# Kernel optimization log

Hardware: AMD Instinct MI355X
Metric: run time of the kernel (lower is better)

The kernel has to match this reference:

```python
import jax, jax.numpy as jnp
import numpy as np


def _ln(z, g, b, eps=1e-5):
    mu = z.mean(-1, keepdims=True)
    v = ((z - mu) ** 2).mean(-1, keepdims=True)
    return (z - mu) / jnp.sqrt(v + eps) * g + b


def _forward(x, C_prev, n_prev, m_prev, ln_in_g, ln_in_b, wq, bq, wk, bk, wv, bv, wi, bi, wf, bf, wo, bo, rd_w1, rd_b1, rd_g, rd_be, rd_w2, rd_b2, ssm_log_lam, ssm_log_b, ssm_c, ssm_log_d, ssm_log_step, ssm_vol_gate, ssm_alpha, ssm_ln_g, ssm_ln_b, ln_mem_g, ln_mem_b):
    B, S, F = x.shape
    D = wq.shape[0]
    sqd = jnp.sqrt(jnp.float32(D))
    w = max(1, int(S * 0.2))
    pad0 = jnp.zeros((B, 1, F), x.dtype)
    cs = jnp.concatenate([pad0, jnp.cumsum(x, 1)], 1)
    cs2 = jnp.concatenate([pad0, jnp.cumsum(x * x, 1)], 1)
    wsum = cs[:, w:] - cs[:, :-w]
    wsq = cs2[:, w:] - cs2[:, :-w]
    var = (wsq - wsum * wsum / w) / (w - 1)
    std = jnp.sqrt(jnp.clip(var, 0.0))
    vol = jnp.concatenate([jnp.broadcast_to(std[:, :1], (B, w - 1, F)), std], 1)
    sv = vol.mean(2, keepdims=True)
    sv = sv / (sv.mean(1, keepdims=True) + 1e-6)  # [B,S,1]
    # --- parallel gate computation ---
    xn = _ln(x, ln_in_g, ln_in_b)
    regime = jax.nn.softmax(jax.nn.gelu(_ln(xn @ rd_w1.T + rd_b1, rd_g, rd_be), approximate=False) @ rd_w2.T + rd_b2, axis=-1)
    q = xn @ wq.T + bq
    k = (xn @ wk.T + bk) / sqd
    v = xn @ wv.T + bv
    it = xn @ wi.T + bi  # [B,S,1]
    ft = xn @ wf.T + bf
    o = jax.nn.sigmoid(xn @ wo.T + bo)
    # --- stabilize_gates (running-max exponential stabilization) ---
    mp = jnp.clip(m_prev, -100.0, 100.0)[:, None, :]  # [B,1,1]
    m_t = jnp.maximum(ft, mp + ft)
    ig = jnp.exp(jnp.clip(it - m_t, -15.0, 15.0))
    fg = jnp.exp(jnp.clip(ft + mp - m_t, -15.0, 15.0))
    # --- store_key_value outer products + cumulative matrix memory ---
    kn = k / (jnp.linalg.norm(k, axis=2, keepdims=True) + 1e-12) * sqd
    vn = v / (jnp.linalg.norm(v, axis=2, keepdims=True) + 1e-6) * sqd
    upd = jnp.clip(ig, 0.0, 1.0)[..., None] * (vn[..., :, None] * kn[..., None, :])  # [B,S,D,D]
    f_cum = jnp.cumprod(fg, axis=1)  # [B,S,1]
    C_t = f_cum[..., None] * C_prev[:, None] + jnp.cumsum(upd, 1)
    # --- structured state-space mixing, vectorized over the D memory rows ---
    lam = -jnp.exp(ssm_log_lam)
    step = jnp.exp(ssm_log_step)
    a_disc = (2.0 + step * lam) / (2.0 - step * lam)  # bilinear discretization
    b_disc = step * (1.0 + a_disc) * jnp.exp(ssm_log_b)[:, 0] / 2.0
    xr = C_t.transpose(0, 2, 1, 3).reshape(B * D, S, D)  # rows folded into batch
    volr = jnp.broadcast_to(sv[:, None, :, 0], (B, D, S)).reshape(B * D, S)
    u = xr.mean(-1)  # [BD,S], per-step scalar drive
    vgate = jax.nn.sigmoid(ssm_vol_gate)
    def stepf(h, inp):
        u_t, vol_t = inp
        h = a_disc[None] * h + b_disc[None] * u_t[:, None]
        h = _ln(h, ssm_ln_g, ssm_ln_b)
        h = h / (1.0 + vgate[None] * vol_t[:, None])
        return h, h
    h0 = jnp.zeros((B * D, D), x.dtype)
    _, hs = jax.lax.scan(stepf, h0, (u.T, volr.T))  # [S,BD,D]
    yscal = jnp.einsum('sbn,n->bs', hs, ssm_c[0])  # [BD,S]
    y = yscal[..., None] + jnp.exp(ssm_log_d) * xr
    alpha = jax.nn.sigmoid(ssm_alpha)
    mixed = alpha * xr + (1.0 - alpha) * y
    C_mixed = mixed.reshape(B, D, S, D).transpose(0, 2, 1, 3)
    mf = regime[:, :, 0:1][..., None]  # regime-aware mixing factor
    C_t = C_mixed * mf + C_t * (1.0 - mf)
    C_t = C_t / (jnp.linalg.norm(C_t.reshape(B, S, D * D), axis=-1)[..., None, None] + 1e-6) * sqd
    # --- mLSTM readout (stabilizer_threshold = 1.0) ---
    n_t = f_cum * n_prev[:, None, :] + jnp.cumsum(ig * k, 1)
    h_til = jnp.einsum('bsij,bsj->bsi', C_t, q)
    denom = jnp.maximum(jnp.abs(jnp.sum(n_t * q, -1, keepdims=True)), 1.0)
    return o * _ln(h_til / denom, ln_mem_g, ln_mem_b)


def setup_inputs() -> dict:
    key = jax.random.key(0)
    ks = jax.random.split(key, 12)
    B, S, F, D = 8, 512, 32, 64
    sF, sD = 1.0 / np.sqrt(F), 1.0 / np.sqrt(D)
    n = lambda k, sh, s=1.0: jax.random.normal(k, sh, jnp.float32) * s
    return dict(
        x=n(ks[0], (B, S, F)),
        C_prev=jnp.zeros((B, D, D), jnp.float32),
        n_prev=jnp.zeros((B, D), jnp.float32),
        m_prev=jnp.zeros((B, 1), jnp.float32),
        ln_in_g=jnp.ones((F,), jnp.float32), ln_in_b=jnp.zeros((F,), jnp.float32),
        wq=n(ks[1], (D, F), sF), bq=jnp.zeros((D,), jnp.float32),
        wk=n(ks[2], (D, F), sF), bk=jnp.zeros((D,), jnp.float32),
        wv=n(ks[3], (D, F), sF), bv=jnp.zeros((D,), jnp.float32),
        wi=n(ks[4], (1, F), sF), bi=jnp.zeros((1,), jnp.float32),
        wf=n(ks[5], (1, F), sF), bf=jnp.ones((1,), jnp.float32),
        wo=n(ks[6], (D, F), sF), bo=jnp.zeros((D,), jnp.float32),
        rd_w1=n(ks[7], (D, F), sF), rd_b1=jnp.zeros((D,), jnp.float32),
        rd_g=jnp.ones((D,), jnp.float32), rd_be=jnp.zeros((D,), jnp.float32),
        rd_w2=n(ks[8], (4, D), sD), rd_b2=jnp.zeros((4,), jnp.float32),
        ssm_log_lam=jnp.linspace(np.log(0.001), np.log(0.1), D).astype(jnp.float32),
        ssm_log_b=jax.random.uniform(ks[9], (D, 1), jnp.float32, -0.5, 0.5),
        ssm_c=n(ks[10], (1, D), sD),
        ssm_log_d=jnp.zeros((1,), jnp.float32),
        ssm_log_step=jnp.float32(np.log(0.001)),
        ssm_vol_gate=jnp.ones((D,), jnp.float32),
        ssm_alpha=jnp.float32(0.7),
        ssm_ln_g=jnp.ones((D,), jnp.float32), ssm_ln_b=jnp.zeros((D,), jnp.float32),
        ln_mem_g=jnp.ones((D,), jnp.float32), ln_mem_b=jnp.zeros((D,), jnp.float32),
    )


def reference(x, C_prev, n_prev, m_prev, ln_in_g, ln_in_b, wq, bq, wk, bk, wv, bv, wi, bi, wf, bf, wo, bo, rd_w1, rd_b1, rd_g, rd_be, rd_w2, rd_b2, ssm_log_lam, ssm_log_b, ssm_c, ssm_log_d, ssm_log_step, ssm_vol_gate, ssm_alpha, ssm_ln_g, ssm_ln_b, ln_mem_g, ln_mem_b):
    return _forward(x, C_prev, n_prev, m_prev, ln_in_g, ln_in_b, wq, bq, wk, bk, wv, bv, wi, bi, wf, bf, wo, bo, rd_w1, rd_b1, rd_g, rd_be, rd_w2, rd_b2, ssm_log_lam, ssm_log_b, ssm_c, ssm_log_d, ssm_log_step, ssm_vol_gate, ssm_alpha, ssm_ln_g, ssm_ln_b, ln_mem_g, ln_mem_b)
```

## Files before the change

kernel.cpp:

```cpp
#include <hip/hip_runtime.h>
#include <math.h>

#define BB 8
#define SS 512
#define FF 32
#define DD 64
#define WVOL 102
#define CH 16
#define NCH (SS / CH)

template<int CTRL, int RM, bool BC>
__device__ __forceinline__ float updpp(float oldv, float x) {
  return __int_as_float(__builtin_amdgcn_update_dpp(
      __float_as_int(oldv), __float_as_int(x), CTRL, RM, 0xF, BC));
}
__device__ __forceinline__ float rlane(float v, int l) {
  return __int_as_float(__builtin_amdgcn_readlane(__float_as_int(v), l));
}
__device__ __forceinline__ float dsum64(float x) {
  x += updpp<0x111, 0xF, true>(0.f, x);
  x += updpp<0x112, 0xF, true>(0.f, x);
  x += updpp<0x114, 0xF, true>(0.f, x);
  x += updpp<0x118, 0xF, true>(0.f, x);
  x += updpp<0x142, 0xF, true>(0.f, x);
  x += updpp<0x143, 0xF, true>(0.f, x);
  return rlane(x, 63);
}
__device__ __forceinline__ float dsum32(float x) {
  x += updpp<0x111, 0xF, true>(0.f, x);
  x += updpp<0x112, 0xF, true>(0.f, x);
  x += updpp<0x114, 0xF, true>(0.f, x);
  x += updpp<0x118, 0xF, true>(0.f, x);
  x += updpp<0x142, 0xF, true>(0.f, x);
  return rlane(x, 31);
}
__device__ __forceinline__ float dsum16(float x) {
  x += updpp<0x111, 0xF, true>(0.f, x);
  x += updpp<0x112, 0xF, true>(0.f, x);
  x += updpp<0x114, 0xF, true>(0.f, x);
  x += updpp<0x118, 0xF, true>(0.f, x);
  return x;
}
__device__ __forceinline__ float dscan_add(float x) {
  x += updpp<0x111, 0xF, true>(0.f, x);
  x += updpp<0x112, 0xF, true>(0.f, x);
  x += updpp<0x114, 0xF, true>(0.f, x);
  x += updpp<0x118, 0xF, true>(0.f, x);
  x += updpp<0x142, 0xA, true>(0.f, x);
  x += updpp<0x143, 0xC, true>(0.f, x);
  return x;
}
__device__ __forceinline__ float dscan_mul(float x) {
  x *= updpp<0x111, 0xF, false>(1.f, x);
  x *= updpp<0x112, 0xF, false>(1.f, x);
  x *= updpp<0x114, 0xF, false>(1.f, x);
  x *= updpp<0x118, 0xF, false>(1.f, x);
  x *= updpp<0x142, 0xA, false>(1.f, x);
  x *= updpp<0x143, 0xC, false>(1.f, x);
  return x;
}

__global__ void k_prep(const float* __restrict__ Cp,
                       const float* __restrict__ wq, const float* __restrict__ wk,
                       const float* __restrict__ wv, const float* __restrict__ wo,
                       const float* __restrict__ rw1,
                       float* __restrict__ CpT, float* __restrict__ wqT,
                       float* __restrict__ wkT, float* __restrict__ wvT,
                       float* __restrict__ woT, float* __restrict__ rw1T,
                       float* __restrict__ cpr, float* __restrict__ cpn2) {
  int blk = blockIdx.x; int lane = threadIdx.x;
  if (blk < BB) {
    int b = blk;
    const float* rowp = Cp + (size_t)(b * DD + lane) * DD;
    float rs = 0.f, r2 = 0.f;
#pragma unroll 8
    for (int j = 0; j < DD; ++j) {
      float c = rowp[j];
      rs += c; r2 = fmaf(c, c, r2);
      CpT[(size_t)(b * DD + j) * DD + lane] = c;
    }
    cpr[b * DD + lane] = rs;
    float tot2 = dsum64(r2);
    if (lane == 0) cpn2[b] = tot2;
  } else {
    const float* src; float* dst;
    switch (blk - BB) {
      case 0: src = wq;  dst = wqT;  break;
      case 1: src = wk;  dst = wkT;  break;
      case 2: src = wv;  dst = wvT;  break;
      case 3: src = wo;  dst = woT;  break;
      default: src = rw1; dst = rw1T; break;
    }
#pragma unroll 8
    for (int f = 0; f < FF; ++f) dst[f * DD + lane] = src[lane * FF + f];
  }
}

__global__ void k_vol_std(const float* __restrict__ x, float* __restrict__ svraw) {
  int b = blockIdx.x; int s = WVOL - 1 + blockIdx.y;
  int lane = threadIdx.x; int f = lane & 31; int half = lane >> 5;
  const float* xb = x + (size_t)(b * SS) * FF + f;
  float wsum = 0.f, wsq = 0.f;
  int t0 = s - WVOL + 1 + half;
#pragma unroll 17
  for (int k = 0; k < WVOL / 2; ++k) {
    float xv = xb[(t0 + 2 * k) * FF];
    wsum += xv; wsq = fmaf(xv, xv, wsq);
  }
  wsum += __shfl_xor(wsum, 32); wsq += __shfl_xor(wsq, 32);
  float var = (wsq - wsum * wsum * (1.f / WVOL)) * (1.f / (WVOL - 1));
  float sd = sqrtf(fmaxf(var, 0.f));
  float m = dsum64(sd) * 0.5f * (1.f / FF);
  if (lane == 0) svraw[b * SS + s] = m;
}

__global__ void k_proj(const float* __restrict__ x, const float* __restrict__ m_prev,
                       const float* __restrict__ CpT,
                       const float* __restrict__ ln_in_g, const float* __restrict__ ln_in_b,
                       const float* __restrict__ wqT, const float* __restrict__ bq,
                       const float* __restrict__ wkT, const float* __restrict__ bk,
                       const float* __restrict__ wvT, const float* __restrict__ bv,
                       const float* __restrict__ wi, const float* __restrict__ bi,
                       const float* __restrict__ wf, const float* __restrict__ bf,
                       const float* __restrict__ woT, const float* __restrict__ bo,
                       const float* __restrict__ rw1T, const float* __restrict__ rd_b1,
                       const float* __restrict__ rd_g, const float* __restrict__ rd_be,
                       const float* __restrict__ rd_w2, const float* __restrict__ rd_b2,
                       float* __restrict__ qo, float* __restrict__ kno, float* __restrict__ vno,
                       float* __restrict__ iko, float* __restrict__ oo,
                       float* __restrict__ cg_a, float* __restrict__ fg_a,
                       float* __restrict__ mf_a, float* __restrict__ cks_a,
                       float* __restrict__ qsum_a, float* __restrict__ zc) {
  int bs = blockIdx.x; int b = bs / SS;
  int lane = threadIdx.x;
  __shared__ float xs[FF];
  __shared__ float ks[DD];
  float xv = (lane < FF) ? x[bs * FF + lane] : 0.f;
  float s1x = dsum32(xv);
  float s2x = dsum32(xv * xv);
  if (lane < FF) {
    float mu = s1x * (1.f / FF);
    float var = s2x * (1.f / FF) - mu * mu;
    xs[lane] = (xv - mu) * rsqrtf(var + 1e-5f) * ln_in_g[lane] + ln_in_b[lane];
  }
  __syncthreads();
  int d = lane;
  float aq = bq[d], ak = bk[d], av = bv[d], ao = bo[d], at = rd_b1[d];
#pragma unroll
  for (int f = 0; f < FF; ++f) {
    float xf = xs[f];
    aq = fmaf(xf, wqT[f * DD + d], aq);
    ak = fmaf(xf, wkT[f * DD + d], ak);
    av = fmaf(xf, wvT[f * DD + d], av);
    ao = fmaf(xf, woT[f * DD + d], ao);
    at = fmaf(xf, rw1T[f * DD + d], at);
  }
  float pit = (lane < FF) ? xs[lane] * wi[lane] : 0.f;
  float pft = (lane < FF) ? xs[lane] * wf[lane] : 0.f;
  float itv = dsum32(pit) + bi[0];
  float ftv = dsum32(pft) + bf[0];
  float s1 = dsum64(at), s2 = dsum64(at * at);
  float mu = s1 * (1.f / DD);
  float var = s2 * (1.f / DD) - mu * mu;
  float tn = (at - mu) * rsqrtf(var + 1e-5f) * rd_g[d] + rd_be[d];
  float ge = 0.5f * tn * (1.f + erff(tn * 0.70710678118654752f));
  float l0 = dsum64(ge * rd_w2[0 * DD + d]) + rd_b2[0];
  float l1 = dsum64(ge * rd_w2[1 * DD + d]) + rd_b2[1];
  float l2 = dsum64(ge * rd_w2[2 * DD + d]) + rd_b2[2];
  float l3 = dsum64(ge * rd_w2[3 * DD + d]) + rd_b2[3];
  float mx = fmaxf(fmaxf(l0, l1), fmaxf(l2, l3));
  float e0 = expf(l0 - mx), e1 = expf(l1 - mx), e2 = expf(l2 - mx), e3 = expf(l3 - mx);
  float mfv = e0 / (e0 + e1 + e2 + e3);
  float kd = ak * 0.125f;
  float kk = dsum64(kd * kd);
  float knd = kd * (8.f / (sqrtf(kk) + 1e-12f));
  float vv = dsum64(av * av);
  float vnd = av * (8.f / (sqrtf(vv) + 1e-6f));
  float ksum = dsum64(knd);
  float qsum = dsum64(aq);
  float mp = fminf(fmaxf(m_prev[b], -100.f), 100.f);
  float mt = fmaxf(ftv, mp + ftv);
  float ig = expf(fminf(fmaxf(itv - mt, -15.f), 15.f));
  float fg = expf(fminf(fmaxf(ftv + mp - mt, -15.f), 15.f));
  float cg = fminf(ig, 1.f);
  qo[bs * DD + d] = aq;
  kno[bs * DD + d] = knd;
  vno[bs * DD + d] = vnd;
  iko[bs * DD + d] = ig * kd;
  oo[bs * DD + d] = 1.f / (1.f + expf(-ao));
  ks[d] = knd;
  __syncthreads();
  float acc = 0.f;
  const float* cpt = CpT + (size_t)b * DD * DD;
#pragma unroll 8
  for (int j = 0; j < DD; ++j) acc = fmaf(cpt[j * DD + d], ks[j], acc);
  float z = dsum64(vnd * acc);
  if (lane == 0) {
    cg_a[bs] = cg; fg_a[bs] = fg; mf_a[bs] = mfv;
    cks_a[bs] = cg * ksum; qsum_a[bs] = qsum;
    zc[bs] = cg * z;
  }
}

__global__ void k_qk(const float* __restrict__ qo, const float* __restrict__ kno,
                     const float* __restrict__ vno, const float* __restrict__ cg_a,
                     float* __restrict__ W, float* __restrict__ rho) {
  int blk = blockIdx.x; int b = blk / 136; int r = blk % 136;
  int st = 0;
  while ((st + 1) * (st + 2) / 2 <= r) ++st;
  int tt = r - st * (st + 1) / 2;
  int s0 = st * 32, t0 = tt * 32;
  int tid = threadIdx.x; int ty = tid >> 4, tx = tid & 15;
  __shared__ float qls[32][64], kls[32][64], vsl[32][64];
  __shared__ float ktl[32][68], vtl[32][68];
  __shared__ float cgl[32], sacc[32];
  {
    int col = tid & 63, rg = tid >> 6;
#pragma unroll
    for (int rr = 0; rr < 8; ++rr) {
      int row = rg * 8 + rr;
      int gi = (b * SS + s0 + row) * DD + col;
      int gj = (b * SS + t0 + row) * DD + col;
      qls[row][col] = qo[gi]; kls[row][col] = kno[gi]; vsl[row][col] = vno[gi];
      ktl[row][col] = kno[gj]; vtl[row][col] = vno[gj];
    }
    if (tid < 32) cgl[tid] = cg_a[b * SS + t0 + tid];
  }
  __syncthreads();
  float A[2][2] = {{0.f, 0.f}, {0.f, 0.f}};
  float KK[2][2] = {{0.f, 0.f}, {0.f, 0.f}};
  float VV[2][2] = {{0.f, 0.f}, {0.f, 0.f}};
  for (int k4 = 0; k4 < DD; k4 += 4) {
    float qa[2][4], ka[2][4], va[2][4], kt[2][4], vt[2][4];
#pragma unroll
    for (int i = 0; i < 2; ++i) {
      float4 t1 = *(const float4*)&qls[ty * 2 + i][k4];
      qa[i][0] = t1.x; qa[i][1] = t1.y; qa[i][2] = t1.z; qa[i][3] = t1.w;
      float4 t2 = *(const float4*)&kls[ty * 2 + i][k4];
      ka[i][0] = t2.x; ka[i][1] = t2.y; ka[i][2] = t2.z; ka[i][3] = t2.w;
      float4 t3 = *(const float4*)&vsl[ty * 2 + i][k4];
      va[i][0] = t3.x; va[i][1] = t3.y; va[i][2] = t3.z; va[i][3] = t3.w;
      float4 t4 = *(const float4*)&ktl[tx * 2 + i][k4];
      kt[i][0] = t4.x; kt[i][1] = t4.y; kt[i][2] = t4.z; kt[i][3] = t4.w;
      float4 t5 = *(const float4*)&vtl[tx * 2 + i][k4];
      vt[i][0] = t5.x; vt[i][1] = t5.y; vt[i][2] = t5.z; vt[i][3] = t5.w;
    }
#pragma unroll
    for (int kk = 0; kk < 4; ++kk)
#pragma unroll
      for (int i = 0; i < 2; ++i)
#pragma unroll
        for (int j = 0; j < 2; ++j) {
          A[i][j]  = fmaf(qa[i][kk], kt[j][kk], A[i][j]);
          KK[i][j] = fmaf(ka[i][kk], kt[j][kk], KK[i][j]);
          VV[i][j] = fmaf(va[i][kk], vt[j][kk], VV[i][j]);
        }
  }
  float cg0 = cgl[tx * 2], cg1 = cgl[tx * 2 + 1];
  int tg0 = t0 + tx * 2, tg1 = t0 + tx * 2 + 1;
#pragma unroll
  for (int i = 0; i < 2; ++i) {
    int s = s0 + ty * 2 + i;
    float w0 = (tg0 <= s) ? cg0 * A[i][0] : 0.f;
    float w1 = (tg1 <= s) ? cg1 * A[i][1] : 0.f;
    float2 wst = make_float2(w0, w1);
    *(float2*)&W[((size_t)b * SS + s) * SS + tg0] = wst;
    float wr0 = (tg0 < s) ? 2.f : (tg0 == s ? 1.f : 0.f);
    float wr1 = (tg1 < s) ? 2.f : (tg1 == s ? 1.f : 0.f);
    float rsum = dsum16(fmaf(wr0 * cg0, KK[i][0] * VV[i][0],
                             wr1 * cg1 * KK[i][1] * VV[i][1]));
    if (tx == 15) sacc[ty * 2 + i] = rsum;
  }
  __syncthreads();
  if (tid < 32) {
    int s = s0 + tid;
    atomicAdd(&rho[b * SS + s], cg_a[b * SS + s] * sacc[tid]);
  }
}

__global__ void k_pv(const float* __restrict__ W, const float* __restrict__ vno,
                     float* __restrict__ p2) {
  int blk = blockIdx.x; int b = blk / 26; int u = blk % 26;
  int st32, c0, c1;
  if (u < 6) { st32 = u; c0 = 0; c1 = u >> 1; }
  else {
    int v = u - 6; st32 = 6 + (v >> 1);
    int nch = (st32 >> 1) + 1; int h0 = nch >> 1;
    if (v & 1) { c0 = h0; c1 = nch - 1; } else { c0 = 0; c1 = h0 - 1; }
  }
  int s0 = st32 * 32;
  int tid = threadIdx.x; int ty = tid >> 4, tx = tid & 15;
  __shared__ float wls[32][64];
  __shared__ float vls[64][64];
  float acc[2][4] = {{0.f, 0.f, 0.f, 0.f}, {0.f, 0.f, 0.f, 0.f}};
  for (int c = c0; c <= c1; ++c) {
    __syncthreads();
    int t0 = c * 64;
    int col = tid & 63, rg = tid >> 6;
#pragma unroll
    for (int rr = 0; rr < 8; ++rr) {
      int r2 = rg * 8 + rr;
      wls[r2][col] = W[((size_t)b * SS + s0 + r2) * SS + t0 + col];
    }
#pragma unroll
    for (int rr = 0; rr < 16; ++rr) {
      int t = rg * 16 + rr;
      vls[t][col] = vno[(b * SS + t0 + t) * DD + col];
    }
    __syncthreads();
    for (int k4 = 0; k4 < 64; k4 += 4) {
      float aa[2][4];
#pragma unroll
      for (int i = 0; i < 2; ++i) {
        float4 t1 = *(const float4*)&wls[ty * 2 + i][k4];
        aa[i][0] = t1.x; aa[i][1] = t1.y; aa[i][2] = t1.z; aa[i][3] = t1.w;
      }
      float bb[4][4];
#pragma unroll
      for (int kk = 0; kk < 4; ++kk) {
        float4 t2 = *(const float4*)&vls[k4 + kk][tx * 4];
        bb[kk][0] = t2.x; bb[kk][1] = t2.y; bb[kk][2] = t2.z; bb[kk][3] = t2.w;
      }
#pragma unroll
      for (int kk = 0; kk < 4; ++kk)
#pragma unroll
        for (int i = 0; i < 2; ++i)
#pragma unroll
          for (int j = 0; j < 4; ++j)
            acc[i][j] = fmaf(aa[i][kk], bb[kk][j], acc[i][j]);
    }
  }
#pragma unroll
  for (int i = 0; i < 2; ++i)
#pragma unroll
    for (int j = 0; j < 4; ++j)
      atomicAdd(&p2[(b * SS + s0 + ty * 2 + i) * DD + tx * 4 + j], acc[i][j]);
}

__global__ void k_post(const float* __restrict__ fg_a, const float* __restrict__ zc,
                       const float* __restrict__ rho, const float* __restrict__ svraw,
                       const float* __restrict__ ik, const float* __restrict__ vno,
                       const float* __restrict__ cks_a,
                       float* __restrict__ fcum, float* __restrict__ cpd,
                       float* __restrict__ sn2, float* __restrict__ sv,
                       float* __restrict__ csn, float* __restrict__ csr) {
  int blk = blockIdx.x; int lane = threadIdx.x;
  if (blk < BB) {
    int b = blk;
    float m0 = svraw[b * SS + WVOL - 1];
    float vals[8]; float part = 0.f;
#pragma unroll
    for (int c = 0; c < 8; ++c) {
      int idx = c * 64 + lane;
      float v = (idx < WVOL - 1) ? m0 : svraw[b * SS + idx];
      vals[c] = v; part += v;
    }
    float tot = dsum64(part);
    float inv = 1.f / (tot * (1.f / SS) + 1e-6f);
#pragma unroll
    for (int c = 0; c < 8; ++c) sv[b * SS + c * 64 + lane] = vals[c] * inv;
    float cf = 1.f, cz = 0.f, crr = 0.f;
    for (int c = 0; c < 8; ++c) {
      int bs = b * SS + c * 64 + lane;
      float f = dscan_mul(fg_a[bs]) * cf;
      float z = dscan_add(zc[bs]) + cz;
      float r = dscan_add(rho[bs]) + crr;
      fcum[bs] = f; cpd[bs] = z; sn2[bs] = r;
      cf = rlane(f, 63); cz = rlane(z, 63); crr = rlane(r, 63);
    }
  } else {
    int blk2 = blk - BB; int b = blk2 / NCH; int w = blk2 % NCH; int d = lane;
    float na = 0.f, ra = 0.f;
#pragma unroll
    for (int t = 0; t < CH; ++t) {
      int bs = b * SS + w * CH + t;
      na += ik[bs * DD + d];
      ra = fmaf(cks_a[bs], vno[bs * DD + d], ra);
    }
    csn[blk2 * DD + d] = na; csr[blk2 * DD + d] = ra;
  }
}

__global__ void k_scan_apply(const float* __restrict__ ik, const float* __restrict__ vno,
                             const float* __restrict__ cks_a,
                             const float* __restrict__ csn, const float* __restrict__ csr,
                             float* __restrict__ nacc, float* __restrict__ racc) {
  int blk = blockIdx.x; int b = blk / NCH; int w = blk % NCH; int d = threadIdx.x;
  float na = 0.f, ra = 0.f;
  for (int w2 = 0; w2 < w; ++w2) {
    na += csn[(b * NCH + w2) * DD + d];
    ra += csr[(b * NCH + w2) * DD + d];
  }
#pragma unroll
  for (int t = 0; t < CH; ++t) {
    int bs = b * SS + w * CH + t;
    na += ik[bs * DD + d];
    ra = fmaf(cks_a[bs], vno[bs * DD + d], ra);
    nacc[bs * DD + d] = na;
    racc[bs * DD + d] = ra;
  }
}

__global__ void k_ssm(const float* __restrict__ fcum, const float* __restrict__ racc,
                      const float* __restrict__ cpr, const float* __restrict__ sv,
                      const float* __restrict__ log_lam, const float* __restrict__ log_b,
                      const float* __restrict__ cvec,
                      const float* __restrict__ log_step, const float* __restrict__ vol_gate,
                      const float* __restrict__ ln_g, const float* __restrict__ ln_b,
                      float* __restrict__ ysT) {
  int blk = blockIdx.x; int b = blk >> 6; int i = blk & 63;
  int n = threadIdx.x;
  float st = expf(log_step[0]);
  float lam = -expf(log_lam[n]);
  float ad = (2.f + st * lam) / (2.f - st * lam);
  float bd = st * (1.f + ad) * expf(log_b[n]) * 0.5f;
  float vg = 1.f / (1.f + expf(-vol_gate[n]));
  float g = ln_g[n], be = ln_b[n], cn = cvec[n];
  float cprv = cpr[b * DD + i];
  float u[8], w[8];
#pragma unroll
  for (int c = 0; c < 8; ++c) {
    int s = c * 64 + n; int bs = b * SS + s;
    u[c] = fmaf(fcum[bs], cprv, racc[(size_t)bs * DD + i]) * (1.f / DD);
    w[c] = sv[bs];
  }
  float h = 0.f;
#pragma unroll
  for (int c = 0; c < 8; ++c) {
    float yout = 0.f;
#pragma unroll 4
    for (int t = 0; t < 64; ++t) {
      float uu = rlane(u[c], t);
      float vv = rlane(w[c], t);
      float bdu = bd * uu;
      float rden = __builtin_amdgcn_rcpf(fmaf(vg, vv, 1.f));
      float grden = g * rden, berden = be * rden;
      float ht = fmaf(ad, h, bdu);
      float p1 = ht, p2 = ht * ht;
      p1 += updpp<0x111, 0xF, true>(0.f, p1); p2 += updpp<0x111, 0xF, true>(0.f, p2);
      p1 += updpp<0x112, 0xF, true>(0.f, p1); p2 += updpp<0x112, 0xF, true>(0.f, p2);
      p1 += updpp<0x114, 0xF, true>(0.f, p1); p2 += updpp<0x114, 0xF, true>(0.f, p2);
      p1 += updpp<0x118, 0xF, true>(0.f, p1); p2 += updpp<0x118, 0xF, true>(0.f, p2);
      p1 += updpp<0x142, 0xF, true>(0.f, p1); p2 += updpp<0x142, 0xF, true>(0.f, p2);
      p1 += updpp<0x143, 0xF, true>(0.f, p1); p2 += updpp<0x143, 0xF, true>(0.f, p2);
      float s1 = rlane(p1, 63), s2 = rlane(p2, 63);
      float mu = s1 * (1.f / DD);
      float r2m = fmaf(-mu, s1, s2);
      float arg = fmaxf(fmaf(r2m, 1.f / DD, 1e-5f), 1e-5f);
      float irs = __builtin_amdgcn_rsqf(arg);
      float hv = fmaf((ht - mu) * grden, irs, berden);
      h = hv;
      float y = cn * hv;
      y += updpp<0x111, 0xF, true>(0.f, y);
      y += updpp<0x112, 0xF, true>(0.f, y);
      y += updpp<0x114, 0xF, true>(0.f, y);
      y += updpp<0x118, 0xF, true>(0.f, y);
      y += updpp<0x142, 0xF, true>(0.f, y);
      y += updpp<0x143, 0xF, true>(0.f, y);
      float su = rlane(y, 63);
      yout = (n == t) ? su : yout;
    }
    ysT[(size_t)(b * DD + i) * SS + c * 64 + n] = yout;
  }
}

__global__ void k_final(const float* __restrict__ qo, const float* __restrict__ oo,
                        const float* __restrict__ p2, const float* __restrict__ racc,
                        const float* __restrict__ nacc, const float* __restrict__ ysT,
                        const float* __restrict__ CpT, const float* __restrict__ cpr,
                        const float* __restrict__ cpn2,
                        const float* __restrict__ fcum, const float* __restrict__ cpd,
                        const float* __restrict__ sn2,
                        const float* __restrict__ mf_a, const float* __restrict__ qsum_a,
                        const float* __restrict__ n_prev,
                        const float* __restrict__ ssm_log_d, const float* __restrict__ ssm_alpha,
                        const float* __restrict__ ln_mem_g, const float* __restrict__ ln_mem_b,
                        float* __restrict__ out) {
  int bs = blockIdx.x; int b = bs / SS; int s = bs % SS;
  int i = threadIdx.x;
  __shared__ float qv[DD];
  float qi = qo[bs * DD + i];
  qv[i] = qi;
  __syncthreads();
  float P1 = 0.f;
  const float* cpt = CpT + (size_t)b * DD * DD;
#pragma unroll 8
  for (int j = 0; j < DD; ++j) P1 = fmaf(cpt[j * DD + i], qv[j], P1);
  float fc = fcum[bs];
  float p = fmaf(fc, P1, p2[bs * DD + i]);
  float r = fmaf(fc, cpr[b * DD + i], racc[bs * DD + i]);
  float R2 = fc * fc * cpn2[b] + 2.f * fc * cpd[bs] + sn2[bs];
  float al = 1.f / (1.f + expf(-ssm_alpha[0]));
  float kap = al + (1.f - al) * expf(ssm_log_d[0]);
  float mfv = mf_a[bs];
  float beta = 1.f + mfv * (kap - 1.f);
  float gam = mfv * (1.f - al);
  float y = ysT[(size_t)(b * DD + i) * SS + s];
  float syr = dsum64(y * r);
  float sy2 = dsum64(y * y);
  float nrm2 = fmaxf(beta * beta * R2 + 2.f * beta * gam * syr + gam * gam * (float)DD * sy2, 0.f);
  float scale = 8.f / (sqrtf(nrm2) + 1e-6f);
  float nt = fmaf(fc, n_prev[b * DD + i], nacc[bs * DD + i]);
  float ndp = dsum64(nt * qi);
  float denom = fmaxf(fabsf(ndp), 1.f);
  float hh = scale * (fmaf(beta, p, gam * y * qsum_a[bs])) / denom;
  float s1 = dsum64(hh), s2 = dsum64(hh * hh);
  float mu = s1 * (1.f / DD);
  float var = fmaxf(s2 * (1.f / DD) - mu * mu, 0.f);
  float o = (hh - mu) * rsqrtf(var + 1e-5f) * ln_mem_g[i] + ln_mem_b[i];
  out[bs * DD + i] = oo[bs * DD + i] * o;
}

extern "C" void kernel_launch(void* const* d_in, const int* in_sizes, int n_in,
                              void* d_out, int out_size, void* d_ws, size_t ws_size,
                              hipStream_t stream) {
  const float* x        = (const float*)d_in[0];
  const float* C_prev   = (const float*)d_in[1];
  const float* n_prev   = (const float*)d_in[2];
  const float* m_prev   = (const float*)d_in[3];
  const float* ln_in_g  = (const float*)d_in[4];
  const float* ln_in_b  = (const float*)d_in[5];
  const float* wq = (const float*)d_in[6];  const float* bq = (const float*)d_in[7];
  const float* wk = (const float*)d_in[8];  const float* bk = (const float*)d_in[9];
  const float* wv = (const float*)d_in[10]; const float* bv = (const float*)d_in[11];
  const float* wi = (const float*)d_in[12]; const float* bi = (const float*)d_in[13];
  const float* wf = (const float*)d_in[14]; const float* bf = (const float*)d_in[15];
  const float* wo = (const float*)d_in[16]; const float* bo = (const float*)d_in[17];
  const float* rd_w1 = (const float*)d_in[18]; const float* rd_b1 = (const float*)d_in[19];
  const float* rd_g  = (const float*)d_in[20]; const float* rd_be = (const float*)d_in[21];
  const float* rd_w2 = (const float*)d_in[22]; const float* rd_b2 = (const float*)d_in[23];
  const float* ssm_log_lam  = (const float*)d_in[24];
  const float* ssm_log_b    = (const float*)d_in[25];
  const float* ssm_c        = (const float*)d_in[26];
  const float* ssm_log_d    = (const float*)d_in[27];
  const float* ssm_log_step = (const float*)d_in[28];
  const float* ssm_vol_gate = (const float*)d_in[29];
  const float* ssm_alpha    = (const float*)d_in[30];
  const float* ssm_ln_g     = (const float*)d_in[31];
  const float* ssm_ln_b     = (const float*)d_in[32];
  const float* ln_mem_g     = (const float*)d_in[33];
  const float* ln_mem_b     = (const float*)d_in[34];
  float* out = (float*)d_out;

  float* Wsp = (float*)d_ws;
  size_t o0 = 0;
  const size_t BS = (size_t)BB * SS, BSD = BS * DD, WSZ = (size_t)BB * SS * SS;
  float* sv    = Wsp + o0; o0 += BS;
  float* svraw = Wsp + o0; o0 += BS;
  float* qo   = Wsp + o0; o0 += BSD;
  float* kno  = Wsp + o0; o0 += BSD;
  float* vno  = Wsp + o0; o0 += BSD;
  float* iko  = Wsp + o0; o0 += BSD;
  float* oo   = Wsp + o0; o0 += BSD;
  float* racc = Wsp + o0; o0 += BSD;
  float* nacc = Wsp + o0; o0 += BSD;
  float* ysT  = Wsp + o0; o0 += BSD;
  float* p2   = Wsp + o0; o0 += BSD;
  float* rho  = Wsp + o0; o0 += BS;
  float* Wm   = Wsp + o0; o0 += WSZ;
  float* cg_a = Wsp + o0; o0 += BS;
  float* fg_a = Wsp + o0; o0 += BS;
  float* mf_a = Wsp + o0; o0 += BS;
  float* cks  = Wsp + o0; o0 += BS;
  float* qsum = Wsp + o0; o0 += BS;
  float* zc   = Wsp + o0; o0 += BS;
  float* fcum = Wsp + o0; o0 += BS;
  float* cpd  = Wsp + o0; o0 += BS;
  float* sn2  = Wsp + o0; o0 += BS;
  float* cpr  = Wsp + o0; o0 += (size_t)BB * DD;
  float* cpn2 = Wsp + o0; o0 += BB;
  float* csn  = Wsp + o0; o0 += (size_t)BB * NCH * DD;
  float* csr  = Wsp + o0; o0 += (size_t)BB * NCH * DD;
  float* CpT  = Wsp + o0; o0 += (size_t)BB * DD * DD;
  float* wqT  = Wsp + o0; o0 += (size_t)FF * DD;
  float* wkT  = Wsp + o0; o0 += (size_t)FF * DD;
  float* wvT  = Wsp + o0; o0 += (size_t)FF * DD;
  float* woT  = Wsp + o0; o0 += (size_t)FF * DD;
  float* rw1T = Wsp + o0; o0 += (size_t)FF * DD;

  hipMemsetAsync(p2, 0, (BSD + BS + WSZ) * sizeof(float), stream);
  hipLaunchKernelGGL(k_prep, dim3(BB + 5), dim3(64), 0, stream,
                     C_prev, wq, wk, wv, wo, rd_w1,
                     CpT, wqT, wkT, wvT, woT, rw1T, cpr, cpn2);
  hipLaunchKernelGGL(k_vol_std, dim3(BB, SS - WVOL + 1), dim3(64), 0, stream, x, svraw);
  hipLaunchKernelGGL(k_proj, dim3(BB * SS), dim3(64), 0, stream,
                     x, m_prev, CpT, ln_in_g, ln_in_b, wqT, bq, wkT, bk, wvT, bv, wi, bi,
                     wf, bf, woT, bo, rw1T, rd_b1, rd_g, rd_be, rd_w2, rd_b2,
                     qo, kno, vno, iko, oo, cg_a, fg_a, mf_a, cks, qsum, zc);
  hipLaunchKernelGGL(k_qk, dim3(BB * 136), dim3(256), 0, stream,
                     qo, kno, vno, cg_a, Wm, rho);
  hipLaunchKernelGGL(k_pv, dim3(BB * 26), dim3(256), 0, stream, Wm, vno, p2);
  hipLaunchKernelGGL(k_post, dim3(BB + BB * NCH), dim3(64), 0, stream,
                     fg_a, zc, rho, svraw, iko, vno, cks,
                     fcum, cpd, sn2, sv, csn, csr);
  hipLaunchKernelGGL(k_scan_apply, dim3(BB * NCH), dim3(64), 0, stream,
                     iko, vno, cks, csn, csr, nacc, racc);
  hipLaunchKernelGGL(k_ssm, dim3(BB * DD), dim3(64), 0, stream,
                     fcum, racc, cpr, sv, ssm_log_lam, ssm_log_b, ssm_c,
                     ssm_log_step, ssm_vol_gate, ssm_ln_g, ssm_ln_b, ysT);
  hipLaunchKernelGGL(k_final, dim3(BB * SS), dim3(64), 0, stream,
                     qo, oo, p2, racc, nacc, ysT, CpT, cpr, cpn2, fcum, cpd, sn2,
                     mf_a, qsum, n_prev, ssm_log_d, ssm_alpha, ln_mem_g, ln_mem_b, out);
}
```

Measured before the change: 295.1 us.

## Restructure SSM recurrence to drop per-step output reduction and batch DPP reductions

The SSM inner loop no longer runs a separate cross-lane reduction for y = c·h at every timestep. The LayerNorm output is expanded algebraically so y comes from the already-reduced mean and rsqrt plus a third fused reduction of (c*g*rden)*h, combined with per-timestep sums S1 and S2. Those sums are precomputed in extra blocks appended to k_scan_apply. Independent DPP reductions in k_proj, k_post and k_final are also interleaved (2/3/4-way) to hide DPP latency. In exchange the kernel adds extra workspace buffers and blocks, and the reassociated math can shift floating-point rounding.

Result: no change. 300.4 us (+1.8%).

```diff
diff --git a/kernel.cpp b/kernel.cpp
--- a/kernel.cpp
+++ b/kernel.cpp
@@ -26,13 +26,40 @@
   x += updpp<0x143, 0xF, true>(0.f, x);
   return rlane(x, 63);
 }
-__device__ __forceinline__ float dsum32(float x) {
-  x += updpp<0x111, 0xF, true>(0.f, x);
-  x += updpp<0x112, 0xF, true>(0.f, x);
-  x += updpp<0x114, 0xF, true>(0.f, x);
-  x += updpp<0x118, 0xF, true>(0.f, x);
-  x += updpp<0x142, 0xF, true>(0.f, x);
-  return rlane(x, 31);
+__device__ __forceinline__ void dred2(float& a, float& b) {
+  a += updpp<0x111,0xF,true>(0.f,a); b += updpp<0x111,0xF,true>(0.f,b);
+  a += updpp<0x112,0xF,true>(0.f,a); b += updpp<0x112,0xF,true>(0.f,b);
+  a += updpp<0x114,0xF,true>(0.f,a); b += updpp<0x114,0xF,true>(0.f,b);
+  a += updpp<0x118,0xF,true>(0.f,a); b += updpp<0x118,0xF,true>(0.f,b);
+  a += updpp<0x142,0xF,true>(0.f,a); b += updpp<0x142,0xF,true>(0.f,b);
+  a += updpp<0x143,0xF,true>(0.f,a); b += updpp<0x143,0xF,true>(0.f,b);
+  a = rlane(a, 63); b = rlane(b, 63);
+}
+__device__ __forceinline__ void dred3(float& a, float& b, float& c) {
+  a += updpp<0x111,0xF,true>(0.f,a); b += updpp<0x111,0xF,true>(0.f,b); c += updpp<0x111,0xF,true>(0.f,c);
+  a += updpp<0x112,0xF,true>(0.f,a); b += updpp<0x112,0xF,true>(0.f,b); c += updpp<0x112,0xF,true>(0.f,c);
+  a += updpp<0x114,0xF,true>(0.f,a); b += updpp<0x114,0xF,true>(0.f,b); c += updpp<0x114,0xF,true>(0.f,c);
+  a += updpp<0x118,0xF,true>(0.f,a); b += updpp<0x118,0xF,true>(0.f,b); c += updpp<0x118,0xF,true>(0.f,c);
+  a += updpp<0x142,0xF,true>(0.f,a); b += updpp<0x142,0xF,true>(0.f,b); c += updpp<0x142,0xF,true>(0.f,c);
+  a += updpp<0x143,0xF,true>(0.f,a); b += updpp<0x143,0xF,true>(0.f,b); c += updpp<0x143,0xF,true>(0.f,c);
+  a = rlane(a, 63); b = rlane(b, 63); c = rlane(c, 63);
+}
+__device__ __forceinline__ void dred4(float& a, float& b, float& c, float& d) {
+  a += updpp<0x111,0xF,true>(0.f,a); b += updpp<0x111,0xF,true>(0.f,b); c += updpp<0x111,0xF,true>(0.f,c); d += updpp<0x111,0xF,true>(0.f,d);
+  a += updpp<0x112,0xF,true>(0.f,a); b += updpp<0x112,0xF,true>(0.f,b); c += updpp<0x112,0xF,true>(0.f,c); d += updpp<0x112,0xF,true>(0.f,d);
+  a += updpp<0x114,0xF,true>(0.f,a); b += updpp<0x114,0xF,true>(0.f,b); c += updpp<0x114,0xF,true>(0.f,c); d += updpp<0x114,0xF,true>(0.f,d);
+  a += updpp<0x118,0xF,true>(0.f,a); b += updpp<0x118,0xF,true>(0.f,b); c += updpp<0x118,0xF,true>(0.f,c); d += updpp<0x118,0xF,true>(0.f,d);
+  a += updpp<0x142,0xF,true>(0.f,a); b += updpp<0x142,0xF,true>(0.f,b); c += updpp<0x142,0xF,true>(0.f,c); d += updpp<0x142,0xF,true>(0.f,d);
+  a += updpp<0x143,0xF,true>(0.f,a); b += updpp<0x143,0xF,true>(0.f,b); c += updpp<0x143,0xF,true>(0.f,c); d += updpp<0x143,0xF,true>(0.f,d);
+  a = rlane(a, 63); b = rlane(b, 63); c = rlane(c, 63); d = rlane(d, 63);
+}
+__device__ __forceinline__ void dred2_32(float& a, float& b) {
+  a += updpp<0x111,0xF,true>(0.f,a); b += updpp<0x111,0xF,true>(0.f,b);
+  a += updpp<0x112,0xF,true>(0.f,a); b += updpp<0x112,0xF,true>(0.f,b);
+  a += updpp<0x114,0xF,true>(0.f,a); b += updpp<0x114,0xF,true>(0.f,b);
+  a += updpp<0x118,0xF,true>(0.f,a); b += updpp<0x118,0xF,true>(0.f,b);
+  a += updpp<0x142,0xF,true>(0.f,a); b += updpp<0x142,0xF,true>(0.f,b);
+  a = rlane(a, 31); b = rlane(b, 31);
 }
 __device__ __forceinline__ float dsum16(float x) {
   x += updpp<0x111, 0xF, true>(0.f, x);
@@ -41,23 +68,13 @@
   x += updpp<0x118, 0xF, true>(0.f, x);
   return x;
 }
-__device__ __forceinline__ float dscan_add(float x) {
-  x += updpp<0x111, 0xF, true>(0.f, x);
-  x += updpp<0x112, 0xF, true>(0.f, x);
-  x += updpp<0x114, 0xF, true>(0.f, x);
-  x += updpp<0x118, 0xF, true>(0.f, x);
-  x += updpp<0x142, 0xA, true>(0.f, x);
-  x += updpp<0x143, 0xC, true>(0.f, x);
-  return x;
-}
-__device__ __forceinline__ float dscan_mul(float x) {
-  x *= updpp<0x111, 0xF, false>(1.f, x);
-  x *= updpp<0x112, 0xF, false>(1.f, x);
-  x *= updpp<0x114, 0xF, false>(1.f, x);
-  x *= updpp<0x118, 0xF, false>(1.f, x);
-  x *= updpp<0x142, 0xA, false>(1.f, x);
-  x *= updpp<0x143, 0xC, false>(1.f, x);
-  return x;
+__device__ __forceinline__ void dscan3(float& f, float& z, float& r) {
+  f *= updpp<0x111,0xF,false>(1.f,f); z += updpp<0x111,0xF,true>(0.f,z); r += updpp<0x111,0xF,true>(0.f,r);
+  f *= updpp<0x112,0xF,false>(1.f,f); z += updpp<0x112,0xF,true>(0.f,z); r += updpp<0x112,0xF,true>(0.f,r);
+  f *= updpp<0x114,0xF,false>(1.f,f); z += updpp<0x114,0xF,true>(0.f,z); r += updpp<0x114,0xF,true>(0.f,r);
+  f *= updpp<0x118,0xF,false>(1.f,f); z += updpp<0x118,0xF,true>(0.f,z); r += updpp<0x118,0xF,true>(0.f,r);
+  f *= updpp<0x142,0xA,false>(1.f,f); z += updpp<0x142,0xA,true>(0.f,z); r += updpp<0x142,0xA,true>(0.f,r);
+  f *= updpp<0x143,0xC,false>(1.f,f); z += updpp<0x143,0xC,true>(0.f,z); r += updpp<0x143,0xC,true>(0.f,r);
 }
 
 __global__ void k_prep(const float* __restrict__ Cp,
@@ -136,8 +153,8 @@
   __shared__ float xs[FF];
   __shared__ float ks[DD];
   float xv = (lane < FF) ? x[bs * FF + lane] : 0.f;
-  float s1x = dsum32(xv);
-  float s2x = dsum32(xv * xv);
+  float s1x = xv, s2x = xv * xv;
+  dred2_32(s1x, s2x);
   if (lane < FF) {
     float mu = s1x * (1.f / FF);
     float var = s2x * (1.f / FF) - mu * mu;
@@ -157,27 +174,28 @@
   }
   float pit = (lane < FF) ? xs[lane] * wi[lane] : 0.f;
   float pft = (lane < FF) ? xs[lane] * wf[lane] : 0.f;
-  float itv = dsum32(pit) + bi[0];
-  float ftv = dsum32(pft) + bf[0];
-  float s1 = dsum64(at), s2 = dsum64(at * at);
+  dred2_32(pit, pft);
+  float itv = pit + bi[0];
+  float ftv = pft + bf[0];
+  float s1 = at, s2 = at * at;
+  dred2(s1, s2);
   float mu = s1 * (1.f / DD);
   float var = s2 * (1.f / DD) - mu * mu;
   float tn = (at - mu) * rsqrtf(var + 1e-5f) * rd_g[d] + rd_be[d];
   float ge = 0.5f * tn * (1.f + erff(tn * 0.70710678118654752f));
-  float l0 = dsum64(ge * rd_w2[0 * DD + d]) + rd_b2[0];
-  float l1 = dsum64(ge * rd_w2[1 * DD + d]) + rd_b2[1];
-  float l2 = dsum64(ge * rd_w2[2 * DD + d]) + rd_b2[2];
-  float l3 = dsum64(ge * rd_w2[3 * DD + d]) + rd_b2[3];
+  float l0 = ge * rd_w2[0 * DD + d], l1 = ge * rd_w2[1 * DD + d];
+  float l2 = ge * rd_w2[2 * DD + d], l3 = ge * rd_w2[3 * DD + d];
+  dred4(l0, l1, l2, l3);
+  l0 += rd_b2[0]; l1 += rd_b2[1]; l2 += rd_b2[2]; l3 += rd_b2[3];
   float mx = fmaxf(fmaxf(l0, l1), fmaxf(l2, l3));
   float e0 = expf(l0 - mx), e1 = expf(l1 - mx), e2 = expf(l2 - mx), e3 = expf(l3 - mx);
   float mfv = e0 / (e0 + e1 + e2 + e3);
   float kd = ak * 0.125f;
-  float kk = dsum64(kd * kd);
+  float kk = kd * kd, vv = av * av, qsum = aq;
+  dred3(kk, vv, qsum);
   float knd = kd * (8.f / (sqrtf(kk) + 1e-12f));
-  float vv = dsum64(av * av);
   float vnd = av * (8.f / (sqrtf(vv) + 1e-6f));
   float ksum = dsum64(knd);
-  float qsum = dsum64(aq);
   float mp = fminf(fmaxf(m_prev[b], -100.f), 100.f);
   float mt = fmaxf(ftv, mp + ftv);
   float ig = expf(fminf(fmaxf(itv - mt, -15.f), 15.f));
@@ -362,9 +380,9 @@
     float cf = 1.f, cz = 0.f, crr = 0.f;
     for (int c = 0; c < 8; ++c) {
       int bs = b * SS + c * 64 + lane;
-      float f = dscan_mul(fg_a[bs]) * cf;
-      float z = dscan_add(zc[bs]) + cz;
-      float r = dscan_add(rho[bs]) + crr;
+      float f = fg_a[bs], z = zc[bs], r = rho[bs];
+      dscan3(f, z, r);
+      f *= cf; z += cz; r += crr;
       fcum[bs] = f; cpd[bs] = z; sn2[bs] = r;
       cf = rlane(f, 63); cz = rlane(z, 63); crr = rlane(r, 63);
     }
@@ -384,20 +402,37 @@
 __global__ void k_scan_apply(const float* __restrict__ ik, const float* __restrict__ vno,
                              const float* __restrict__ cks_a,
                              const float* __restrict__ csn, const float* __restrict__ csr,
-                             float* __restrict__ nacc, float* __restrict__ racc) {
-  int blk = blockIdx.x; int b = blk / NCH; int w = blk % NCH; int d = threadIdx.x;
-  float na = 0.f, ra = 0.f;
-  for (int w2 = 0; w2 < w; ++w2) {
-    na += csn[(b * NCH + w2) * DD + d];
-    ra += csr[(b * NCH + w2) * DD + d];
-  }
-#pragma unroll
-  for (int t = 0; t < CH; ++t) {
-    int bs = b * SS + w * CH + t;
-    na += ik[bs * DD + d];
-    ra = fmaf(cks_a[bs], vno[bs * DD + d], ra);
-    nacc[bs * DD + d] = na;
-    racc[bs * DD + d] = ra;
+                             const float* __restrict__ sv,
+                             const float* __restrict__ cvec, const float* __restrict__ ln_g,
+                             const float* __restrict__ ln_b, const float* __restrict__ vol_gate,
+                             float* __restrict__ nacc, float* __restrict__ racc,
+                             float* __restrict__ S1g, float* __restrict__ S2g) {
+  int blk = blockIdx.x;
+  if (blk < BB * NCH) {
+    int b = blk / NCH; int w = blk % NCH; int d = threadIdx.x;
+    float na = 0.f, ra = 0.f;
+    for (int w2 = 0; w2 < w; ++w2) {
+      na += csn[(b * NCH + w2) * DD + d];
+      ra += csr[(b * NCH + w2) * DD + d];
+    }
+#pragma unroll
+    for (int t = 0; t < CH; ++t) {
+      int bs = b * SS + w * CH + t;
+      na += ik[bs * DD + d];
+      ra = fmaf(cks_a[bs], vno[bs * DD + d], ra);
+      nacc[bs * DD + d] = na;
+      racc[bs * DD + d] = ra;
+    }
+  } else {
+    int bs = blk - BB * NCH;
+    int nn = threadIdx.x;
+    float cn = cvec[nn], g = ln_g[nn], be = ln_b[nn];
+    float vg = 1.f / (1.f + expf(-vol_gate[nn]));
+    float vol = sv[bs];
+    float rden = __builtin_amdgcn_rcpf(fmaf(vg, vol, 1.f));
+    float r1 = cn * g * rden, r2 = cn * be * rden;
+    dred2(r1, r2);
+    if (nn == 0) { S1g[bs] = r1; S2g[bs] = r2; }
   }
 }
 
@@ -407,6 +442,7 @@
                       const float* __restrict__ cvec,
                       const float* __restrict__ log_step, const float* __restrict__ vol_gate,
                       const float* __restrict__ ln_g, const float* __restrict__ ln_b,
+                      const float* __restrict__ S1g, const float* __restrict__ S2g,
                       float* __restrict__ ysT) {
   int blk = blockIdx.x; int b = blk >> 6; int i = blk & 63;
   int n = threadIdx.x;
@@ -416,51 +452,48 @@
   float bd = st * (1.f + ad) * expf(log_b[n]) * 0.5f;
   float vg = 1.f / (1.f + expf(-vol_gate[n]));
   float g = ln_g[n], be = ln_b[n], cn = cvec[n];
+  float adg = ad * g, adbe = ad * be, cng = cn * g;
   float cprv = cpr[b * DD + i];
-  float u[8], w[8];
+  float u[8], w[8], S1a[8], S2a[8];
 #pragma unroll
   for (int c = 0; c < 8; ++c) {
     int s = c * 64 + n; int bs = b * SS + s;
     u[c] = fmaf(fcum[bs], cprv, racc[(size_t)bs * DD + i]) * (1.f / DD);
     w[c] = sv[bs];
-  }
-  float h = 0.f;
+    S1a[c] = S1g[bs]; S2a[c] = S2g[bs];
+  }
+  float ht = bd * rlane(u[0], 0);
 #pragma unroll
   for (int c = 0; c < 8; ++c) {
-    float yout = 0.f;
+    float macc = 0.f, iacc = 0.f, s3acc = 0.f;
 #pragma unroll 4
-    for (int t = 0; t < 64; ++t) {
-      float uu = rlane(u[c], t);
-      float vv = rlane(w[c], t);
-      float bdu = bd * uu;
-      float rden = __builtin_amdgcn_rcpf(fmaf(vg, vv, 1.f));
-      float grden = g * rden, berden = be * rden;
-      float ht = fmaf(ad, h, bdu);
-      float p1 = ht, p2 = ht * ht;
-      p1 += updpp<0x111, 0xF, true>(0.f, p1); p2 += updpp<0x111, 0xF, true>(0.f, p2);
-      p1 += updpp<0x112, 0xF, true>(0.f, p1); p2 += updpp<0x112, 0xF, true>(0.f, p2);
-      p1 += updpp<0x114, 0xF, true>(0.f, p1); p2 += updpp<0x114, 0xF, true>(0.f, p2);
-      p1 += updpp<0x118, 0xF, true>(0.f, p1); p2 += updpp<0x118, 0xF, true>(0.f, p2);
-      p1 += updpp<0x142, 0xF, true>(0.f, p1); p2 += updpp<0x142, 0xF, true>(0.f, p2);
-      p1 += updpp<0x143, 0xF, true>(0.f, p1); p2 += updpp<0x143, 0xF, true>(0.f, p2);
-      float s1 = rlane(p1, 63), s2 = rlane(p2, 63);
+    for (int t2 = 0; t2 < 64; ++t2) {
+      float vvol = rlane(w[c], t2);
+      float rden = __builtin_amdgcn_rcpf(fmaf(vg, vvol, 1.f));
+      float p1 = ht, p2 = ht * ht, p3 = (cng * rden) * ht;
+      p1 += updpp<0x111,0xF,true>(0.f,p1); p2 += updpp<0x111,0xF,true>(0.f,p2); p3 += updpp<0x111,0xF,true>(0.f,p3);
+      p1 += updpp<0x112,0xF,true>(0.f,p1); p2 += updpp<0x112,0xF,true>(0.f,p2); p3 += updpp<0x112,0xF,true>(0.f,p3);
+      p1 += updpp<0x114,0xF,true>(0.f,p1); p2 += updpp<0x114,0xF,true>(0.f,p2); p3 += updpp<0x114,0xF,true>(0.f,p3);
+      p1 += updpp<0x118,0xF,true>(0.f,p1); p2 += updpp<0x118,0xF,true>(0.f,p2); p3 += updpp<0x118,0xF,true>(0.f,p3);
+      p1 += updpp<0x142,0xF,true>(0.f,p1); p2 += updpp<0x142,0xF,true>(0.f,p2); p3 += updpp<0x142,0xF,true>(0.f,p3);
+      p1 += updpp<0x143,0xF,true>(0.f,p1); p2 += updpp<0x143,0xF,true>(0.f,p2); p3 += updpp<0x143,0xF,true>(0.f,p3);
+      float s1 = rlane(p1, 63), s2v = rlane(p2, 63), s3 = rlane(p3, 63);
       float mu = s1 * (1.f / DD);
-      float r2m = fmaf(-mu, s1, s2);
+      float r2m = fmaf(-mu, s1, s2v);
       float arg = fmaxf(fmaf(r2m, 1.f / DD, 1e-5f), 1e-5f);
       float irs = __builtin_amdgcn_rsqf(arg);
-      float hv = fmaf((ht - mu) * grden, irs, berden);
-      h = hv;
-      float y = cn * hv;
-      y += updpp<0x111, 0xF, true>(0.f, y);
-      y += updpp<0x112, 0xF, true>(0.f, y);
-      y += updpp<0x114, 0xF, true>(0.f, y);
-      y += updpp<0x118, 0xF, true>(0.f, y);
-      y += updpp<0x142, 0xF, true>(0.f, y);
-      y += updpp<0x143, 0xF, true>(0.f, y);
-      float su = rlane(y, 63);
-      yout = (n == t) ? su : yout;
-    }
-    ysT[(size_t)(b * DD + i) * SS + c * 64 + n] = yout;
+      bool sel = (n == t2);
+      macc = sel ? mu : macc;
+      iacc = sel ? irs : iacc;
+      s3acc = sel ? s3 : s3acc;
+      float un = (t2 < 63) ? rlane(u[c], t2 + 1)
+                           : ((c < 7) ? rlane(u[(c + 1) & 7], 0) : 0.f);
+      float A = adg * rden;
+      float B = fmaf(adbe, rden, bd * un);
+      ht = fmaf((ht - mu) * A, irs, B);
+    }
+    float y = fmaf(iacc, fmaf(-macc, S1a[c], s3acc), S2a[c]);
+    ysT[(size_t)(b * DD + i) * SS + c * 64 + n] = y;
   }
 }
 
@@ -496,15 +529,15 @@
   float beta = 1.f + mfv * (kap - 1.f);
   float gam = mfv * (1.f - al);
   float y = ysT[(size_t)(b * DD + i) * SS + s];
-  float syr = dsum64(y * r);
-  float sy2 = dsum64(y * y);
+  float nt = fmaf(fc, n_prev[b * DD + i], nacc[bs * DD + i]);
+  float syr = y * r, sy2 = y * y, ndp = nt * qi;
+  dred3(syr, sy2, ndp);
   float nrm2 = fmaxf(beta * beta * R2 + 2.f * beta * gam * syr + gam * gam * (float)DD * sy2, 0.f);
   float scale = 8.f / (sqrtf(nrm2) + 1e-6f);
-  float nt = fmaf(fc, n_prev[b * DD + i], nacc[bs * DD + i]);
-  float ndp = dsum64(nt * qi);
   float denom = fmaxf(fabsf(ndp), 1.f);
   float hh = scale * (fmaf(beta, p, gam * y * qsum_a[bs])) / denom;
-  float s1 = dsum64(hh), s2 = dsum64(hh * hh);
+  float s1 = hh, s2 = hh * hh;
+  dred2(s1, s2);
   float mu = s1 * (1.f / DD);
   float var = fmaxf(s2 * (1.f / DD) - mu * mu, 0.f);
   float o = (hh - mu) * rsqrtf(var + 1e-5f) * ln_mem_g[i] + ln_mem_b[i];
@@ -567,6 +600,8 @@
   float* fcum = Wsp + o0; o0 += BS;
   float* cpd  = Wsp + o0; o0 += BS;
   float* sn2  = Wsp + o0; o0 += BS;
+  float* S1g  = Wsp + o0; o0 += BS;
+  float* S2g  = Wsp + o0; o0 += BS;
   float* cpr  = Wsp + o0; o0 += (size_t)BB * DD;
   float* cpn2 = Wsp + o0; o0 += BB;
   float* csn  = Wsp + o0; o0 += (size_t)BB * NCH * DD;
@@ -593,11 +628,12 @@
   hipLaunchKernelGGL(k_post, dim3(BB + BB * NCH), dim3(64), 0, stream,
                      fg_a, zc, rho, svraw, iko, vno, cks,
                      fcum, cpd, sn2, sv, csn, csr);
-  hipLaunchKernelGGL(k_scan_apply, dim3(BB * NCH), dim3(64), 0, stream,
-                     iko, vno, cks, csn, csr, nacc, racc);
+  hipLaunchKernelGGL(k_scan_apply, dim3(BB * NCH + BB * SS), dim3(64), 0, stream,
+                     iko, vno, cks, csn, csr, sv, ssm_c, ssm_ln_g, ssm_ln_b,
+                     ssm_vol_gate, nacc, racc, S1g, S2g);
   hipLaunchKernelGGL(k_ssm, dim3(BB * DD), dim3(64), 0, stream,
                      fcum, racc, cpr, sv, ssm_log_lam, ssm_log_b, ssm_c,
-                     ssm_log_step, ssm_vol_gate, ssm_ln_g, ssm_ln_b, ysT);
+                     ssm_log_step, ssm_vol_gate, ssm_ln_g, ssm_ln_b, S1g, S2g, ysT);
   hipLaunchKernelGGL(k_final, dim3(BB * SS), dim3(64), 0, stream,
                      qo, oo, p2, racc, nacc, ysT, CpT, cpr, cpn2, fcum, cpd, sn2,
                      mf_a, qsum, n_prev, ssm_log_d, ssm_alpha, ln_mem_g, ln_mem_b, out);
```
